# Kernel tuning notes

Measured on AMD Instinct MI355X. Metric: run time of the kernel, lower is better.

## Reference

```python
import jax, jax.numpy as jnp
import numpy as np

B, T_IN, H, IN, OUT, T_DEC = 32768, 20, 128, 2, 2, 45


def lstm_cell(x, h, c, Wih, Whh, bih, bhh):
    # PyTorch gate order: i, f, g, o
    gates = x @ Wih.T + h @ Whh.T + (bih + bhh)
    i, f, g, o = jnp.split(gates, 4, axis=-1)
    c = jax.nn.sigmoid(f) * c + jax.nn.sigmoid(i) * jnp.tanh(g)
    h = jax.nn.sigmoid(o) * jnp.tanh(c)
    return h, c


def lstm_layer(xs, Wih, Whh, bih, bhh):
    # xs: [T, B, in] -> outputs [T, B, H], final (h, c)
    Bsz = xs.shape[1]
    h0 = jnp.zeros((Bsz, H), xs.dtype)
    c0 = jnp.zeros((Bsz, H), xs.dtype)

    def step(carry, x):
        h, c = carry
        h, c = lstm_cell(x, h, c, Wih, Whh, bih, bhh)
        return (h, c), h

    (h, c), ys = jax.lax.scan(step, (h0, c0), xs)
    return ys, h, c


def setup_inputs() -> dict:
    key = jax.random.key(0)
    ks = jax.random.split(key, 20)
    s = 0.05
    d = {
        'input_seq': jax.random.normal(ks[0], (B, T_IN, IN), jnp.float32),
        'enc_Wih0': jax.random.normal(ks[1], (4 * H, IN), jnp.float32) * s,
        'enc_Whh0': jax.random.normal(ks[2], (4 * H, H), jnp.float32) * s,
        'enc_bih0': jax.random.normal(ks[3], (4 * H,), jnp.float32) * s,
        'enc_bhh0': jax.random.normal(ks[4], (4 * H,), jnp.float32) * s,
        'enc_Wih1': jax.random.normal(ks[5], (4 * H, H), jnp.float32) * s,
        'enc_Whh1': jax.random.normal(ks[6], (4 * H, H), jnp.float32) * s,
        'enc_bih1': jax.random.normal(ks[7], (4 * H,), jnp.float32) * s,
        'enc_bhh1': jax.random.normal(ks[8], (4 * H,), jnp.float32) * s,
        'dec_Wih0': jax.random.normal(ks[9], (4 * H, OUT), jnp.float32) * s,
        'dec_Whh0': jax.random.normal(ks[10], (4 * H, H), jnp.float32) * s,
        'dec_bih0': jax.random.normal(ks[11], (4 * H,), jnp.float32) * s,
        'dec_bhh0': jax.random.normal(ks[12], (4 * H,), jnp.float32) * s,
        'dec_Wih1': jax.random.normal(ks[13], (4 * H, H), jnp.float32) * s,
        'dec_Whh1': jax.random.normal(ks[14], (4 * H, H), jnp.float32) * s,
        'dec_bih1': jax.random.normal(ks[15], (4 * H,), jnp.float32) * s,
        'dec_bhh1': jax.random.normal(ks[16], (4 * H,), jnp.float32) * s,
        'fc_W': jax.random.normal(ks[17], (OUT, H), jnp.float32) * s,
        'fc_b': jax.random.normal(ks[18], (OUT,), jnp.float32) * s,
        'target_len': T_DEC,
    }
    return d


def reference(input_seq, enc_Wih0, enc_Whh0, enc_bih0, enc_bhh0,
              enc_Wih1, enc_Whh1, enc_bih1, enc_bhh1,
              dec_Wih0, dec_Whh0, dec_bih0, dec_bhh0,
              dec_Wih1, dec_Whh1, dec_bih1, dec_bhh1,
              fc_W, fc_b, target_len):
    xs = jnp.swapaxes(input_seq, 0, 1)  # [T, B, IN]
    # Encoder: 2 stacked LSTM layers; keep final (h, c) of each layer.
    ys0, h0, c0 = lstm_layer(xs, enc_Wih0, enc_Whh0, enc_bih0, enc_bhh0)
    _, h1, c1 = lstm_layer(ys0, enc_Wih1, enc_Whh1, enc_bih1, enc_bhh1)

    x0 = input_seq[:, -1, :]  # [B, OUT] last observed point

    def dec_step(carry, _):
        hh0, cc0, hh1, cc1, x = carry
        hh0, cc0 = lstm_cell(x, hh0, cc0, dec_Wih0, dec_Whh0, dec_bih0, dec_bhh0)
        hh1, cc1 = lstm_cell(hh0, hh1, cc1, dec_Wih1, dec_Whh1, dec_bih1, dec_bhh1)
        pred = hh1 @ fc_W.T + fc_b  # [B, OUT]
        return (hh0, cc0, hh1, cc1, pred), pred

    _, preds = jax.lax.scan(dec_step, (h0, c0, h1, c1, x0), None, length=target_len)
    return jnp.swapaxes(preds, 0, 1)  # [B, target_len, OUT]
```

## Files before the change

kernel.cpp:

```cpp
#include <hip/hip_runtime.h>

typedef unsigned int u32;
typedef unsigned short u16;
typedef __attribute__((ext_vector_type(8))) short short8;
typedef __attribute__((ext_vector_type(4))) float floatx4;

#define L2E  1.44269504088896340736f
#define L2E2 2.88539008177792681472f

static __device__ __forceinline__ u16 f2bf(float f){
  u32 u = __float_as_uint(f);
  u = (u + 0x7FFFu + ((u >> 16) & 1u)) >> 16;
  return (u16)u;
}
static __device__ __forceinline__ float rcp_(float x){ return __builtin_amdgcn_rcpf(x); }
static __device__ __forceinline__ float exp2_(float x){ return __builtin_amdgcn_exp2f(x); }
static __device__ __forceinline__ float sigm2(float yh){ return rcp_(1.f + exp2_(-yh)); }
static __device__ __forceinline__ float tanh2(float yh2){ return 1.f - 2.f*rcp_(1.f + exp2_(yh2)); }

__global__ __launch_bounds__(256) void prep_weights(
    const float* eWhh0, const float* eWhh1, const float* eWih1,
    const float* dWhh0, const float* dWhh1, const float* dWih1,
    u16* wE0, u16* wE1h, u16* wE1x, u16* wD0, u16* wD1h, u16* wD1x)
{
  int idx = blockIdx.x * 256 + threadIdx.x;
  int m = idx >> 16, e = idx & 65535;
  int j = e & 7, L = (e >> 3) & 63, c = (e >> 9) & 3, g = (e >> 11) & 3, s = (e >> 13) & 7;
  int row = g*128 + s*16 + (L & 15);
  int col = c*32 + ((L >> 4) * 8) + j;
  float scale = (g == 2) ? L2E2 : L2E;
  const float* src; u16* dst;
  switch(m){
    case 0: src = eWhh0; dst = wE0;  break;
    case 1: src = eWhh1; dst = wE1h; break;
    case 2: src = eWih1; dst = wE1x; break;
    case 3: src = dWhh0; dst = wD0;  break;
    case 4: src = dWhh1; dst = wD1h; break;
    default:src = dWih1; dst = wD1x; break;
  }
  dst[e] = f2bf(src[row*128 + col] * scale);
}

__global__ __launch_bounds__(256) void prep_small(
    const float* ebih0,const float* ebhh0,const float* ebih1,const float* ebhh1,
    const float* dbih0,const float* dbhh0,const float* dbih1,const float* dbhh1,
    const float* eWih0,const float* dWih0, float* biasAll, float* wxAll)
{
  int i = blockIdx.x*256 + threadIdx.x;
  if (i < 2048){
    int l = i >> 9, n = i & 511, g = (n >> 7) & 3;
    const float* a = l==0?ebih0: l==1?ebih1: l==2?dbih0: dbih1;
    const float* b = l==0?ebhh0: l==1?ebhh1: l==2?dbhh0: dbhh1;
    biasAll[i] = (a[n] + b[n]) * ((g==2)? L2E2 : L2E);
  } else {
    int k = i - 2048;
    int l = k >> 10, e2 = k & 1023, n = e2 >> 1, g = (n >> 7) & 3;
    const float* wsrc = l ? dWih0 : eWih0;
    wxAll[k] = wsrc[e2] * ((g==2)? L2E2 : L2E);
  }
}

template<bool DEC>
static __device__ __forceinline__ void step_t(
    int grp, int mtb, int lane, int n4, int q, int m0, int t,
    u16* h0s, u16* h1s, float* fcp,
    const float* sB, const float* sWx, const float* sFc,
    const u16* __restrict__ W0, const u16* __restrict__ W1h, const u16* __restrict__ W1x,
    short8 (&ah)[2][4], float2 (&xc)[2][4],
    floatx4 (&c0a)[2][4], floatx4 (&c1a)[2][4],
    float* __restrict__ out)
{
  const int bofs = DEC ? 1024 : 0;
  const int wxo  = DEC ? 512  : 0;

  short8 a1[2][4];
  #pragma unroll
  for (int j = 0; j < 2; j++)
    #pragma unroll
    for (int c = 0; c < 4; c++)
      a1[j][c] = *(const short8*)(h1s + ((mtb+j)*4 + c)*512 + lane*8);

  #pragma unroll 1
  for (int i = 0; i < 4; i++){
    const int s = grp*4 + i;
    const u16* bs = W0 + s*8192;
    short8 bw[4][4];
    #pragma unroll
    for (int c = 0; c < 4; c++)
      #pragma unroll
      for (int g = 0; g < 4; g++)
        bw[g][c] = *(const short8*)(bs + (g*4 + c)*512 + lane*8);
    floatx4 acc[4][2];
    #pragma unroll
    for (int g = 0; g < 4; g++){
      float bi = sB[bofs + g*128 + s*16 + n4];
      float2 wv = ((const float2*)sWx)[wxo + g*128 + s*16 + n4];
      #pragma unroll
      for (int j = 0; j < 2; j++)
        #pragma unroll
        for (int r = 0; r < 4; r++)
          acc[g][j][r] = fmaf(xc[j][r].y, wv.y, fmaf(xc[j][r].x, wv.x, bi));
    }
    #pragma unroll
    for (int c = 0; c < 4; c++)
      #pragma unroll
      for (int g = 0; g < 4; g++){
        acc[g][0] = __builtin_amdgcn_mfma_f32_16x16x32_bf16(ah[0][c], bw[g][c], acc[g][0], 0,0,0);
        acc[g][1] = __builtin_amdgcn_mfma_f32_16x16x32_bf16(ah[1][c], bw[g][c], acc[g][1], 0,0,0);
      }
    #pragma unroll
    for (int j = 0; j < 2; j++){
      const int hb = ((mtb+j)*4 + (s>>1))*512 + ((s&1)*2 + (n4>>3))*128 + q*32 + (n4&7);
      floatx4 cc = c0a[j][i], cn;
      #pragma unroll
      for (int r = 0; r < 4; r++){
        float ig = sigm2(acc[0][j][r]);
        float fg = sigm2(acc[1][j][r]);
        float gg = tanh2(acc[2][j][r]);
        float cv = fmaf(fg, cc[r], ig*gg);
        float og = sigm2(acc[3][j][r]);
        float hv = og * (1.f - 2.f*rcp_(1.f + exp2_(L2E2*cv)));
        cn[r] = cv;
        h0s[hb + r*8] = f2bf(hv);
      }
      c0a[j][i] = cn;
    }
  }
  __syncthreads();

  #pragma unroll
  for (int j = 0; j < 2; j++)
    #pragma unroll
    for (int c = 0; c < 4; c++)
      ah[j][c] = *(const short8*)(h0s + ((mtb+j)*4 + c)*512 + lane*8);

  float p[2][4][2];
  if (DEC){
    #pragma unroll
    for (int j = 0; j < 2; j++)
      #pragma unroll
      for (int r = 0; r < 4; r++){ p[j][r][0] = 0.f; p[j][r][1] = 0.f; }
  }

  #pragma unroll 1
  for (int i = 0; i < 4; i++){
    const int s = grp*4 + i;
    floatx4 acc[4][2];
    #pragma unroll
    for (int g = 0; g < 4; g++){
      float bi = sB[bofs + 512 + g*128 + s*16 + n4];
      #pragma unroll
      for (int j = 0; j < 2; j++)
        #pragma unroll
        for (int r = 0; r < 4; r++) acc[g][j][r] = bi;
    }
    {
      const u16* bs = W1h + s*8192;
      short8 bw[4][4];
      #pragma unroll
      for (int c = 0; c < 4; c++)
        #pragma unroll
        for (int g = 0; g < 4; g++)
          bw[g][c] = *(const short8*)(bs + (g*4 + c)*512 + lane*8);
      #pragma unroll
      for (int c = 0; c < 4; c++)
        #pragma unroll
        for (int g = 0; g < 4; g++){
          acc[g][0] = __builtin_amdgcn_mfma_f32_16x16x32_bf16(a1[0][c], bw[g][c], acc[g][0], 0,0,0);
          acc[g][1] = __builtin_amdgcn_mfma_f32_16x16x32_bf16(a1[1][c], bw[g][c], acc[g][1], 0,0,0);
        }
    }
    {
      const u16* bs = W1x + s*8192;
      short8 bw[4][4];
      #pragma unroll
      for (int c = 0; c < 4; c++)
        #pragma unroll
        for (int g = 0; g < 4; g++)
          bw[g][c] = *(const short8*)(bs + (g*4 + c)*512 + lane*8);
      #pragma unroll
      for (int c = 0; c < 4; c++)
        #pragma unroll
        for (int g = 0; g < 4; g++){
          acc[g][0] = __builtin_amdgcn_mfma_f32_16x16x32_bf16(ah[0][c], bw[g][c], acc[g][0], 0,0,0);
          acc[g][1] = __builtin_amdgcn_mfma_f32_16x16x32_bf16(ah[1][c], bw[g][c], acc[g][1], 0,0,0);
        }
    }
    float f0 = 0.f, f1 = 0.f;
    if (DEC){ f0 = sFc[s*16 + n4]; f1 = sFc[128 + s*16 + n4]; }
    #pragma unroll
    for (int j = 0; j < 2; j++){
      const int hb = ((mtb+j)*4 + (s>>1))*512 + ((s&1)*2 + (n4>>3))*128 + q*32 + (n4&7);
      floatx4 cc = c1a[j][i], cn;
      #pragma unroll
      for (int r = 0; r < 4; r++){
        float ig = sigm2(acc[0][j][r]);
        float fg = sigm2(acc[1][j][r]);
        float gg = tanh2(acc[2][j][r]);
        float cv = fmaf(fg, cc[r], ig*gg);
        float og = sigm2(acc[3][j][r]);
        float hv = og * (1.f - 2.f*rcp_(1.f + exp2_(L2E2*cv)));
        cn[r] = cv;
        h1s[hb + r*8] = f2bf(hv);
        if (DEC){
          p[j][r][0] = fmaf(hv, f0, p[j][r][0]);
          p[j][r][1] = fmaf(hv, f1, p[j][r][1]);
        }
      }
      c1a[j][i] = cn;
    }
  }

  if (DEC){
    #pragma unroll
    for (int off = 1; off < 16; off <<= 1)
      #pragma unroll
      for (int j = 0; j < 2; j++)
        #pragma unroll
        for (int r = 0; r < 4; r++){
          p[j][r][0] += __shfl_xor(p[j][r][0], off);
          p[j][r][1] += __shfl_xor(p[j][r][1], off);
        }
    if (n4 == 0){
      #pragma unroll
      for (int j = 0; j < 2; j++)
        #pragma unroll
        for (int r = 0; r < 4; r++){
          const int base = ((mtb+j)*16 + q*4 + r)*4 + grp*2;
          fcp[base + 0] = p[j][r][0];
          fcp[base + 1] = p[j][r][1];
        }
    }
  }
  __syncthreads();

  if (DEC){
    const float fb0 = sFc[256], fb1 = sFc[257];
    #pragma unroll
    for (int j = 0; j < 2; j++)
      #pragma unroll
      for (int r = 0; r < 4; r++){
        const int base = ((mtb+j)*16 + q*4 + r)*4;
        float2 pv;
        pv.x = fcp[base + 0] + fcp[base + 2] + fb0;
        pv.y = fcp[base + 1] + fcp[base + 3] + fb1;
        xc[j][r] = pv;
        if (grp == 0 && n4 == 0)
          *(float2*)(out + (long)(m0 + (mtb+j)*16 + q*4 + r)*90 + (t - 20)*2) = pv;
      }
  }
}

__global__ __launch_bounds__(512, 1) void lstm_all(
    const float* __restrict__ in_seq,
    const u16* __restrict__ wE0, const u16* __restrict__ wE1h, const u16* __restrict__ wE1x,
    const u16* __restrict__ wD0, const u16* __restrict__ wD1h, const u16* __restrict__ wD1x,
    const float* __restrict__ biasAll, const float* __restrict__ wxAll,
    const float* __restrict__ fcW, const float* __restrict__ fcb,
    float* __restrict__ out)
{
  __shared__ u16 h0s[16384];
  __shared__ u16 h1s[16384];
  __shared__ float sB[2048];
  __shared__ float sWx[2048];
  __shared__ float sFc[260];
  __shared__ float fcp[512];

  const int tid = threadIdx.x, lane = tid & 63, w = tid >> 6;
  const int grp = w >> 2, mtb = (w & 3) * 2;
  const int n4 = lane & 15, q = lane >> 4;
  const int m0 = blockIdx.x * 128;

  for (int i = tid; i < 2048; i += 512){ sB[i] = biasAll[i]; sWx[i] = wxAll[i]; }
  if (tid < 258) sFc[tid] = (tid < 256) ? fcW[tid] : fcb[tid - 256];
  { u32* z0 = (u32*)h0s; u32* z1 = (u32*)h1s;
    for (int i = tid; i < 8192; i += 512){ z0[i] = 0u; z1[i] = 0u; } }

  floatx4 c0a[2][4], c1a[2][4];
  const floatx4 z4 = {0.f,0.f,0.f,0.f};
  #pragma unroll
  for (int j = 0; j < 2; j++)
    #pragma unroll
    for (int i = 0; i < 4; i++){ c0a[j][i] = z4; c1a[j][i] = z4; }
  __syncthreads();

  short8 ah[2][4];
  #pragma unroll
  for (int j = 0; j < 2; j++)
    #pragma unroll
    for (int c = 0; c < 4; c++)
      ah[j][c] = *(const short8*)(h0s + ((mtb+j)*4 + c)*512 + lane*8);
  __syncthreads();

  float2 xc[2][4];

  #pragma unroll 1
  for (int t = 0; t < 20; t++){
    #pragma unroll
    for (int j = 0; j < 2; j++)
      #pragma unroll
      for (int r = 0; r < 4; r++)
        xc[j][r] = *(const float2*)(in_seq + (long)(m0 + (mtb+j)*16 + q*4 + r)*40 + t*2);
    step_t<false>(grp, mtb, lane, n4, q, m0, t, h0s, h1s, fcp, sB, sWx, sFc,
                  wE0, wE1h, wE1x, ah, xc, c0a, c1a, out);
  }

  #pragma unroll
  for (int j = 0; j < 2; j++)
    #pragma unroll
    for (int r = 0; r < 4; r++)
      xc[j][r] = *(const float2*)(in_seq + (long)(m0 + (mtb+j)*16 + q*4 + r)*40 + 38);

  #pragma unroll 1
  for (int t = 20; t < 65; t++){
    step_t<true>(grp, mtb, lane, n4, q, m0, t, h0s, h1s, fcp, sB, sWx, sFc,
                 wD0, wD1h, wD1x, ah, xc, c0a, c1a, out);
  }
}

extern "C" void kernel_launch(void* const* d_in, const int* in_sizes, int n_in,
                              void* d_out, int out_size, void* d_ws, size_t ws_size,
                              hipStream_t stream)
{
  const float* in_seq = (const float*)d_in[0];
  const float* eWih0 = (const float*)d_in[1];
  const float* eWhh0 = (const float*)d_in[2];
  const float* ebih0 = (const float*)d_in[3];
  const float* ebhh0 = (const float*)d_in[4];
  const float* eWih1 = (const float*)d_in[5];
  const float* eWhh1 = (const float*)d_in[6];
  const float* ebih1 = (const float*)d_in[7];
  const float* ebhh1 = (const float*)d_in[8];
  const float* dWih0 = (const float*)d_in[9];
  const float* dWhh0 = (const float*)d_in[10];
  const float* dbih0 = (const float*)d_in[11];
  const float* dbhh0 = (const float*)d_in[12];
  const float* dWih1 = (const float*)d_in[13];
  const float* dWhh1 = (const float*)d_in[14];
  const float* dbih1 = (const float*)d_in[15];
  const float* dbhh1 = (const float*)d_in[16];
  const float* fcW   = (const float*)d_in[17];
  const float* fcb   = (const float*)d_in[18];
  float* out = (float*)d_out;
  char* ws = (char*)d_ws;

  u16* wE0   = (u16*)(ws + 0);
  u16* wE1h  = (u16*)(ws + 131072);
  u16* wE1x  = (u16*)(ws + 262144);
  u16* wD0   = (u16*)(ws + 393216);
  u16* wD1h  = (u16*)(ws + 524288);
  u16* wD1x  = (u16*)(ws + 655360);
  float* biasAll = (float*)(ws + 786432);
  float* wxAll   = (float*)(ws + 794624);

  hipLaunchKernelGGL(prep_weights, dim3(1536), dim3(256), 0, stream,
                     eWhh0, eWhh1, eWih1, dWhh0, dWhh1, dWih1,
                     wE0, wE1h, wE1x, wD0, wD1h, wD1x);
  hipLaunchKernelGGL(prep_small, dim3(16), dim3(256), 0, stream,
                     ebih0, ebhh0, ebih1, ebhh1, dbih0, dbhh0, dbih1, dbhh1,
                     eWih0, dWih0, biasAll, wxAll);

  hipLaunchKernelGGL(lstm_all, dim3(256), dim3(512), 0, stream,
                     in_seq, (const u16*)wE0, (const u16*)wE1h, (const u16*)wE1x,
                     (const u16*)wD0, (const u16*)wD1h, (const u16*)wD1x,
                     (const float*)biasAll, (const float*)wxAll, fcW, fcb, out);
}
```

Baseline: 1.413 ms.

## Software-pipeline weight fragment loads one MFMA block ahead across steps

Measured after the change: 1.705 ms. 1.21x slower.

```diff
diff --git a/kernel.cpp b/kernel.cpp
--- a/kernel.cpp
+++ b/kernel.cpp
@@ -65,31 +65,26 @@
     int grp, int mtb, int lane, int n4, int q, int m0, int t,
     u16* h0s, u16* h1s, float* fcp,
     const float* sB, const float* sWx, const float* sFc,
-    const u16* __restrict__ W0, const u16* __restrict__ W1h, const u16* __restrict__ W1x,
-    short8 (&ah)[2][4], float2 (&xc)[2][4],
+    const u16* __restrict__ W0, const u16* __restrict__ W1h,
+    const u16* __restrict__ W1x, const u16* __restrict__ W0next,
+    short8 (&pf)[16], short8 (&ah)[2][4], float2 (&xc)[2][4],
     floatx4 (&c0a)[2][4], floatx4 (&c1a)[2][4],
     float* __restrict__ out)
 {
   const int bofs = DEC ? 1024 : 0;
   const int wxo  = DEC ? 512  : 0;
+  const int lb = lane * 8;
 
   short8 a1[2][4];
   #pragma unroll
   for (int j = 0; j < 2; j++)
     #pragma unroll
     for (int c = 0; c < 4; c++)
-      a1[j][c] = *(const short8*)(h1s + ((mtb+j)*4 + c)*512 + lane*8);
+      a1[j][c] = *(const short8*)(h1s + ((mtb+j)*4 + c)*512 + lb);
 
   #pragma unroll 1
   for (int i = 0; i < 4; i++){
     const int s = grp*4 + i;
-    const u16* bs = W0 + s*8192;
-    short8 bw[4][4];
-    #pragma unroll
-    for (int c = 0; c < 4; c++)
-      #pragma unroll
-      for (int g = 0; g < 4; g++)
-        bw[g][c] = *(const short8*)(bs + (g*4 + c)*512 + lane*8);
     floatx4 acc[4][2];
     #pragma unroll
     for (int g = 0; g < 4; g++){
@@ -105,9 +100,13 @@
     for (int c = 0; c < 4; c++)
       #pragma unroll
       for (int g = 0; g < 4; g++){
-        acc[g][0] = __builtin_amdgcn_mfma_f32_16x16x32_bf16(ah[0][c], bw[g][c], acc[g][0], 0,0,0);
-        acc[g][1] = __builtin_amdgcn_mfma_f32_16x16x32_bf16(ah[1][c], bw[g][c], acc[g][1], 0,0,0);
-      }
+        acc[g][0] = __builtin_amdgcn_mfma_f32_16x16x32_bf16(ah[0][c], pf[g*4+c], acc[g][0], 0,0,0);
+        acc[g][1] = __builtin_amdgcn_mfma_f32_16x16x32_bf16(ah[1][c], pf[g*4+c], acc[g][1], 0,0,0);
+      }
+    { const u16* nxt = (i < 3) ? (W0 + (s+1)*8192) : (W1h + (grp*4)*8192);
+      #pragma unroll
+      for (int k = 0; k < 16; k++)
+        pf[k] = *(const short8*)(nxt + k*512 + lb); }
     #pragma unroll
     for (int j = 0; j < 2; j++){
       const int hb = ((mtb+j)*4 + (s>>1))*512 + ((s&1)*2 + (n4>>3))*128 + q*32 + (n4&7);
@@ -132,7 +131,7 @@
   for (int j = 0; j < 2; j++)
     #pragma unroll
     for (int c = 0; c < 4; c++)
-      ah[j][c] = *(const short8*)(h0s + ((mtb+j)*4 + c)*512 + lane*8);
+      ah[j][c] = *(const short8*)(h0s + ((mtb+j)*4 + c)*512 + lb);
 
   float p[2][4][2];
   if (DEC){
@@ -154,38 +153,31 @@
         #pragma unroll
         for (int r = 0; r < 4; r++) acc[g][j][r] = bi;
     }
-    {
-      const u16* bs = W1h + s*8192;
-      short8 bw[4][4];
-      #pragma unroll
-      for (int c = 0; c < 4; c++)
-        #pragma unroll
-        for (int g = 0; g < 4; g++)
-          bw[g][c] = *(const short8*)(bs + (g*4 + c)*512 + lane*8);
-      #pragma unroll
-      for (int c = 0; c < 4; c++)
-        #pragma unroll
-        for (int g = 0; g < 4; g++){
-          acc[g][0] = __builtin_amdgcn_mfma_f32_16x16x32_bf16(a1[0][c], bw[g][c], acc[g][0], 0,0,0);
-          acc[g][1] = __builtin_amdgcn_mfma_f32_16x16x32_bf16(a1[1][c], bw[g][c], acc[g][1], 0,0,0);
-        }
-    }
-    {
-      const u16* bs = W1x + s*8192;
-      short8 bw[4][4];
-      #pragma unroll
-      for (int c = 0; c < 4; c++)
-        #pragma unroll
-        for (int g = 0; g < 4; g++)
-          bw[g][c] = *(const short8*)(bs + (g*4 + c)*512 + lane*8);
-      #pragma unroll
-      for (int c = 0; c < 4; c++)
-        #pragma unroll
-        for (int g = 0; g < 4; g++){
-          acc[g][0] = __builtin_amdgcn_mfma_f32_16x16x32_bf16(ah[0][c], bw[g][c], acc[g][0], 0,0,0);
-          acc[g][1] = __builtin_amdgcn_mfma_f32_16x16x32_bf16(ah[1][c], bw[g][c], acc[g][1], 0,0,0);
-        }
-    }
+    #pragma unroll
+    for (int c = 0; c < 4; c++)
+      #pragma unroll
+      for (int g = 0; g < 4; g++){
+        acc[g][0] = __builtin_amdgcn_mfma_f32_16x16x32_bf16(a1[0][c], pf[g*4+c], acc[g][0], 0,0,0);
+        acc[g][1] = __builtin_amdgcn_mfma_f32_16x16x32_bf16(a1[1][c], pf[g*4+c], acc[g][1], 0,0,0);
+      }
+    { const u16* nxt = W1x + s*8192;
+      #pragma unroll
+      for (int k = 0; k < 16; k++)
+        pf[k] = *(const short8*)(nxt + k*512 + lb); }
+    #pragma unroll
+    for (int c = 0; c < 4; c++)
+      #pragma unroll
+      for (int g = 0; g < 4; g++){
+        acc[g][0] = __builtin_amdgcn_mfma_f32_16x16x32_bf16(ah[0][c], pf[g*4+c], acc[g][0], 0,0,0);
+        acc[g][1] = __builtin_amdgcn_mfma_f32_16x16x32_bf16(ah[1][c], pf[g*4+c], acc[g][1], 0,0,0);
+      }
+    { const u16* nxt = (i < 3) ? (W1h + (s+1)*8192)
+                               : (W0next ? (W0next + (grp*4)*8192) : (const u16*)nullptr);
+      if (nxt){
+        #pragma unroll
+        for (int k = 0; k < 16; k++)
+          pf[k] = *(const short8*)(nxt + k*512 + lb);
+      } }
     float f0 = 0.f, f1 = 0.f;
     if (DEC){ f0 = sFc[s*16 + n4]; f1 = sFc[128 + s*16 + n4]; }
     #pragma unroll
@@ -282,6 +274,12 @@
   for (int j = 0; j < 2; j++)
     #pragma unroll
     for (int i = 0; i < 4; i++){ c0a[j][i] = z4; c1a[j][i] = z4; }
+
+  short8 pf[16];
+  { const u16* p0 = wE0 + (grp*4)*8192 + lane*8;
+    #pragma unroll
+    for (int k = 0; k < 16; k++)
+      pf[k] = *(const short8*)(p0 + k*512); }
   __syncthreads();
 
   short8 ah[2][4];
@@ -302,7 +300,8 @@
       for (int r = 0; r < 4; r++)
         xc[j][r] = *(const float2*)(in_seq + (long)(m0 + (mtb+j)*16 + q*4 + r)*40 + t*2);
     step_t<false>(grp, mtb, lane, n4, q, m0, t, h0s, h1s, fcp, sB, sWx, sFc,
-                  wE0, wE1h, wE1x, ah, xc, c0a, c1a, out);
+                  wE0, wE1h, wE1x, (t < 19) ? wE0 : wD0,
+                  pf, ah, xc, c0a, c1a, out);
   }
 
   #pragma unroll
@@ -314,7 +313,8 @@
   #pragma unroll 1
   for (int t = 20; t < 65; t++){
     step_t<true>(grp, mtb, lane, n4, q, m0, t, h0s, h1s, fcp, sB, sWx, sFc,
-                 wD0, wD1h, wD1x, ah, xc, c0a, c1a, out);
+                 wD0, wD1h, wD1x, (t < 64) ? wD0 : (const u16*)nullptr,
+                 pf, ah, xc, c0a, c1a, out);
   }
 }
 
```

## Halve per-block batch tile to 64 rows for higher occupancy

Applied to the files above, without the earlier changes.

After: 2.314 ms. +63.8%, slower.

```diff
diff --git a/kernel.cpp b/kernel.cpp
--- a/kernel.cpp
+++ b/kernel.cpp
@@ -62,152 +62,130 @@
 
 template<bool DEC>
 static __device__ __forceinline__ void step_t(
-    int grp, int mtb, int lane, int n4, int q, int m0, int t,
+    int grp, int mt, int lane, int n4, int q, int m0, int t,
     u16* h0s, u16* h1s, float* fcp,
     const float* sB, const float* sWx, const float* sFc,
-    const u16* __restrict__ W0, const u16* __restrict__ W1h, const u16* __restrict__ W1x,
-    short8 (&ah)[2][4], float2 (&xc)[2][4],
-    floatx4 (&c0a)[2][4], floatx4 (&c1a)[2][4],
+    const u16* __restrict__ W0, const u16* __restrict__ W1h,
+    const u16* __restrict__ W1x,
+    short8 (&ah)[4], float2 (&xc)[4],
+    floatx4 (&c0a)[4], floatx4 (&c1a)[4],
     float* __restrict__ out)
 {
   const int bofs = DEC ? 1024 : 0;
   const int wxo  = DEC ? 512  : 0;
-
-  short8 a1[2][4];
-  #pragma unroll
-  for (int j = 0; j < 2; j++)
-    #pragma unroll
-    for (int c = 0; c < 4; c++)
-      a1[j][c] = *(const short8*)(h1s + ((mtb+j)*4 + c)*512 + lane*8);
+  const int lb = lane * 8;
+
+  short8 a1[4];
+  #pragma unroll
+  for (int c = 0; c < 4; c++)
+    a1[c] = *(const short8*)(h1s + (mt*4 + c)*512 + lb);
 
   #pragma unroll 1
   for (int i = 0; i < 4; i++){
     const int s = grp*4 + i;
     const u16* bs = W0 + s*8192;
-    short8 bw[4][4];
-    #pragma unroll
-    for (int c = 0; c < 4; c++)
-      #pragma unroll
-      for (int g = 0; g < 4; g++)
-        bw[g][c] = *(const short8*)(bs + (g*4 + c)*512 + lane*8);
-    floatx4 acc[4][2];
+    short8 bw[16];
+    #pragma unroll
+    for (int k = 0; k < 16; k++)
+      bw[k] = *(const short8*)(bs + k*512 + lb);
+    floatx4 acc[4];
     #pragma unroll
     for (int g = 0; g < 4; g++){
       float bi = sB[bofs + g*128 + s*16 + n4];
       float2 wv = ((const float2*)sWx)[wxo + g*128 + s*16 + n4];
       #pragma unroll
-      for (int j = 0; j < 2; j++)
-        #pragma unroll
-        for (int r = 0; r < 4; r++)
-          acc[g][j][r] = fmaf(xc[j][r].y, wv.y, fmaf(xc[j][r].x, wv.x, bi));
+      for (int r = 0; r < 4; r++)
+        acc[g][r] = fmaf(xc[r].y, wv.y, fmaf(xc[r].x, wv.x, bi));
     }
     #pragma unroll
     for (int c = 0; c < 4; c++)
       #pragma unroll
-      for (int g = 0; g < 4; g++){
-        acc[g][0] = __builtin_amdgcn_mfma_f32_16x16x32_bf16(ah[0][c], bw[g][c], acc[g][0], 0,0,0);
-        acc[g][1] = __builtin_amdgcn_mfma_f32_16x16x32_bf16(ah[1][c], bw[g][c], acc[g][1], 0,0,0);
-      }
-    #pragma unroll
-    for (int j = 0; j < 2; j++){
-      const int hb = ((mtb+j)*4 + (s>>1))*512 + ((s&1)*2 + (n4>>3))*128 + q*32 + (n4&7);
-      floatx4 cc = c0a[j][i], cn;
+      for (int g = 0; g < 4; g++)
+        acc[g] = __builtin_amdgcn_mfma_f32_16x16x32_bf16(ah[c], bw[g*4+c], acc[g], 0,0,0);
+    {
+      const int hb = (mt*4 + (s>>1))*512 + ((s&1)*2 + (n4>>3))*128 + q*32 + (n4&7);
+      floatx4 cc = c0a[i], cn;
       #pragma unroll
       for (int r = 0; r < 4; r++){
-        float ig = sigm2(acc[0][j][r]);
-        float fg = sigm2(acc[1][j][r]);
-        float gg = tanh2(acc[2][j][r]);
+        float ig = sigm2(acc[0][r]);
+        float fg = sigm2(acc[1][r]);
+        float gg = tanh2(acc[2][r]);
         float cv = fmaf(fg, cc[r], ig*gg);
-        float og = sigm2(acc[3][j][r]);
+        float og = sigm2(acc[3][r]);
         float hv = og * (1.f - 2.f*rcp_(1.f + exp2_(L2E2*cv)));
         cn[r] = cv;
         h0s[hb + r*8] = f2bf(hv);
       }
-      c0a[j][i] = cn;
+      c0a[i] = cn;
     }
   }
   __syncthreads();
 
   #pragma unroll
-  for (int j = 0; j < 2; j++)
-    #pragma unroll
-    for (int c = 0; c < 4; c++)
-      ah[j][c] = *(const short8*)(h0s + ((mtb+j)*4 + c)*512 + lane*8);
-
-  float p[2][4][2];
+  for (int c = 0; c < 4; c++)
+    ah[c] = *(const short8*)(h0s + (mt*4 + c)*512 + lb);
+
+  float p[4][2];
   if (DEC){
     #pragma unroll
-    for (int j = 0; j < 2; j++)
-      #pragma unroll
-      for (int r = 0; r < 4; r++){ p[j][r][0] = 0.f; p[j][r][1] = 0.f; }
+    for (int r = 0; r < 4; r++){ p[r][0] = 0.f; p[r][1] = 0.f; }
   }
 
   #pragma unroll 1
   for (int i = 0; i < 4; i++){
     const int s = grp*4 + i;
-    floatx4 acc[4][2];
+    floatx4 acc[4];
     #pragma unroll
     for (int g = 0; g < 4; g++){
       float bi = sB[bofs + 512 + g*128 + s*16 + n4];
       #pragma unroll
-      for (int j = 0; j < 2; j++)
-        #pragma unroll
-        for (int r = 0; r < 4; r++) acc[g][j][r] = bi;
+      for (int r = 0; r < 4; r++) acc[g][r] = bi;
     }
     {
       const u16* bs = W1h + s*8192;
-      short8 bw[4][4];
+      short8 bw[16];
+      #pragma unroll
+      for (int k = 0; k < 16; k++)
+        bw[k] = *(const short8*)(bs + k*512 + lb);
       #pragma unroll
       for (int c = 0; c < 4; c++)
         #pragma unroll
         for (int g = 0; g < 4; g++)
-          bw[g][c] = *(const short8*)(bs + (g*4 + c)*512 + lane*8);
-      #pragma unroll
-      for (int c = 0; c < 4; c++)
-        #pragma unroll
-        for (int g = 0; g < 4; g++){
-          acc[g][0] = __builtin_amdgcn_mfma_f32_16x16x32_bf16(a1[0][c], bw[g][c], acc[g][0], 0,0,0);
-          acc[g][1] = __builtin_amdgcn_mfma_f32_16x16x32_bf16(a1[1][c], bw[g][c], acc[g][1], 0,0,0);
-        }
+          acc[g] = __builtin_amdgcn_mfma_f32_16x16x32_bf16(a1[c], bw[g*4+c], acc[g], 0,0,0);
     }
     {
       const u16* bs = W1x + s*8192;
-      short8 bw[4][4];
+      short8 bw[16];
+      #pragma unroll
+      for (int k = 0; k < 16; k++)
+        bw[k] = *(const short8*)(bs + k*512 + lb);
       #pragma unroll
       for (int c = 0; c < 4; c++)
         #pragma unroll
         for (int g = 0; g < 4; g++)
-          bw[g][c] = *(const short8*)(bs + (g*4 + c)*512 + lane*8);
-      #pragma unroll
-      for (int c = 0; c < 4; c++)
-        #pragma unroll
-        for (int g = 0; g < 4; g++){
-          acc[g][0] = __builtin_amdgcn_mfma_f32_16x16x32_bf16(ah[0][c], bw[g][c], acc[g][0], 0,0,0);
-          acc[g][1] = __builtin_amdgcn_mfma_f32_16x16x32_bf16(ah[1][c], bw[g][c], acc[g][1], 0,0,0);
-        }
+          acc[g] = __builtin_amdgcn_mfma_f32_16x16x32_bf16(ah[c], bw[g*4+c], acc[g], 0,0,0);
     }
     float f0 = 0.f, f1 = 0.f;
     if (DEC){ f0 = sFc[s*16 + n4]; f1 = sFc[128 + s*16 + n4]; }
-    #pragma unroll
-    for (int j = 0; j < 2; j++){
-      const int hb = ((mtb+j)*4 + (s>>1))*512 + ((s&1)*2 + (n4>>3))*128 + q*32 + (n4&7);
-      floatx4 cc = c1a[j][i], cn;
+    {
+      const int hb = (mt*4 + (s>>1))*512 + ((s&1)*2 + (n4>>3))*128 + q*32 + (n4&7);
+      floatx4 cc = c1a[i], cn;
       #pragma unroll
       for (int r = 0; r < 4; r++){
-        float ig = sigm2(acc[0][j][r]);
-        float fg = sigm2(acc[1][j][r]);
-        float gg = tanh2(acc[2][j][r]);
+        float ig = sigm2(acc[0][r]);
+        float fg = sigm2(acc[1][r]);
+        float gg = tanh2(acc[2][r]);
         float cv = fmaf(fg, cc[r], ig*gg);
-        float og = sigm2(acc[3][j][r]);
+        float og = sigm2(acc[3][r]);
         float hv = og * (1.f - 2.f*rcp_(1.f + exp2_(L2E2*cv)));
         cn[r] = cv;
         h1s[hb + r*8] = f2bf(hv);
         if (DEC){
-          p[j][r][0] = fmaf(hv, f0, p[j][r][0]);
-          p[j][r][1] = fmaf(hv, f1, p[j][r][1]);
+          p[r][0] = fmaf(hv, f0, p[r][0]);
+          p[r][1] = fmaf(hv, f1, p[r][1]);
         }
       }
-      c1a[j][i] = cn;
+      c1a[i] = cn;
     }
   }
 
@@ -215,21 +193,17 @@
     #pragma unroll
     for (int off = 1; off < 16; off <<= 1)
       #pragma unroll
-      for (int j = 0; j < 2; j++)
-        #pragma unroll
-        for (int r = 0; r < 4; r++){
-          p[j][r][0] += __shfl_xor(p[j][r][0], off);
-          p[j][r][1] += __shfl_xor(p[j][r][1], off);
-        }
+      for (int r = 0; r < 4; r++){
+        p[r][0] += __shfl_xor(p[r][0], off);
+        p[r][1] += __shfl_xor(p[r][1], off);
+      }
     if (n4 == 0){
       #pragma unroll
-      for (int j = 0; j < 2; j++)
-        #pragma unroll
-        for (int r = 0; r < 4; r++){
-          const int base = ((mtb+j)*16 + q*4 + r)*4 + grp*2;
-          fcp[base + 0] = p[j][r][0];
-          fcp[base + 1] = p[j][r][1];
-        }
+      for (int r = 0; r < 4; r++){
+        const int base = (mt*16 + q*4 + r)*4 + grp*2;
+        fcp[base + 0] = p[r][0];
+        fcp[base + 1] = p[r][1];
+      }
     }
   }
   __syncthreads();
@@ -237,21 +211,19 @@
   if (DEC){
     const float fb0 = sFc[256], fb1 = sFc[257];
     #pragma unroll
-    for (int j = 0; j < 2; j++)
-      #pragma unroll
-      for (int r = 0; r < 4; r++){
-        const int base = ((mtb+j)*16 + q*4 + r)*4;
-        float2 pv;
-        pv.x = fcp[base + 0] + fcp[base + 2] + fb0;
-        pv.y = fcp[base + 1] + fcp[base + 3] + fb1;
-        xc[j][r] = pv;
-        if (grp == 0 && n4 == 0)
-          *(float2*)(out + (long)(m0 + (mtb+j)*16 + q*4 + r)*90 + (t - 20)*2) = pv;
-      }
-  }
-}
-
-__global__ __launch_bounds__(512, 1) void lstm_all(
+    for (int r = 0; r < 4; r++){
+      const int base = (mt*16 + q*4 + r)*4;
+      float2 pv;
+      pv.x = fcp[base + 0] + fcp[base + 2] + fb0;
+      pv.y = fcp[base + 1] + fcp[base + 3] + fb1;
+      xc[r] = pv;
+      if (grp == 0 && n4 == 0)
+        *(float2*)(out + (long)(m0 + mt*16 + q*4 + r)*90 + (t - 20)*2) = pv;
+    }
+  }
+}
+
+__global__ __launch_bounds__(512, 4) void lstm_all(
     const float* __restrict__ in_seq,
     const u16* __restrict__ wE0, const u16* __restrict__ wE1h, const u16* __restrict__ wE1x,
     const u16* __restrict__ wD0, const u16* __restrict__ wD1h, const u16* __restrict__ wD1x,
@@ -259,61 +231,53 @@
     const float* __restrict__ fcW, const float* __restrict__ fcb,
     float* __restrict__ out)
 {
-  __shared__ u16 h0s[16384];
-  __shared__ u16 h1s[16384];
+  __shared__ u16 h0s[8192];
+  __shared__ u16 h1s[8192];
   __shared__ float sB[2048];
   __shared__ float sWx[2048];
   __shared__ float sFc[260];
-  __shared__ float fcp[512];
+  __shared__ float fcp[256];
 
   const int tid = threadIdx.x, lane = tid & 63, w = tid >> 6;
-  const int grp = w >> 2, mtb = (w & 3) * 2;
+  const int grp = w >> 2, mt = w & 3;
   const int n4 = lane & 15, q = lane >> 4;
-  const int m0 = blockIdx.x * 128;
+  const int m0 = blockIdx.x * 64;
 
   for (int i = tid; i < 2048; i += 512){ sB[i] = biasAll[i]; sWx[i] = wxAll[i]; }
   if (tid < 258) sFc[tid] = (tid < 256) ? fcW[tid] : fcb[tid - 256];
   { u32* z0 = (u32*)h0s; u32* z1 = (u32*)h1s;
-    for (int i = tid; i < 8192; i += 512){ z0[i] = 0u; z1[i] = 0u; } }
-
-  floatx4 c0a[2][4], c1a[2][4];
+    for (int i = tid; i < 4096; i += 512){ z0[i] = 0u; z1[i] = 0u; } }
+
+  floatx4 c0a[4], c1a[4];
   const floatx4 z4 = {0.f,0.f,0.f,0.f};
   #pragma unroll
-  for (int j = 0; j < 2; j++)
-    #pragma unroll
-    for (int i = 0; i < 4; i++){ c0a[j][i] = z4; c1a[j][i] = z4; }
+  for (int i = 0; i < 4; i++){ c0a[i] = z4; c1a[i] = z4; }
   __syncthreads();
 
-  short8 ah[2][4];
-  #pragma unroll
-  for (int j = 0; j < 2; j++)
-    #pragma unroll
-    for (int c = 0; c < 4; c++)
-      ah[j][c] = *(const short8*)(h0s + ((mtb+j)*4 + c)*512 + lane*8);
+  short8 ah[4];
+  #pragma unroll
+  for (int c = 0; c < 4; c++)
+    ah[c] = *(const short8*)(h0s + (mt*4 + c)*512 + lane*8);
   __syncthreads();
 
-  float2 xc[2][4];
+  float2 xc[4];
 
   #pragma unroll 1
   for (int t = 0; t < 20; t++){
     #pragma unroll
-    for (int j = 0; j < 2; j++)
-      #pragma unroll
-      for (int r = 0; r < 4; r++)
-        xc[j][r] = *(const float2*)(in_seq + (long)(m0 + (mtb+j)*16 + q*4 + r)*40 + t*2);
-    step_t<false>(grp, mtb, lane, n4, q, m0, t, h0s, h1s, fcp, sB, sWx, sFc,
+    for (int r = 0; r < 4; r++)
+      xc[r] = *(const float2*)(in_seq + (long)(m0 + mt*16 + q*4 + r)*40 + t*2);
+    step_t<false>(grp, mt, lane, n4, q, m0, t, h0s, h1s, fcp, sB, sWx, sFc,
                   wE0, wE1h, wE1x, ah, xc, c0a, c1a, out);
   }
 
   #pragma unroll
-  for (int j = 0; j < 2; j++)
-    #pragma unroll
-    for (int r = 0; r < 4; r++)
-      xc[j][r] = *(const float2*)(in_seq + (long)(m0 + (mtb+j)*16 + q*4 + r)*40 + 38);
+  for (int r = 0; r < 4; r++)
+    xc[r] = *(const float2*)(in_seq + (long)(m0 + mt*16 + q*4 + r)*40 + 38);
 
   #pragma unroll 1
   for (int t = 20; t < 65; t++){
-    step_t<true>(grp, mtb, lane, n4, q, m0, t, h0s, h1s, fcp, sB, sWx, sFc,
+    step_t<true>(grp, mt, lane, n4, q, m0, t, h0s, h1s, fcp, sB, sWx, sFc,
                  wD0, wD1h, wD1x, ah, xc, c0a, c1a, out);
   }
 }
@@ -360,7 +324,7 @@
                      ebih0, ebhh0, ebih1, ebhh1, dbih0, dbhh0, dbih1, dbhh1,
                      eWih0, dWih0, biasAll, wxAll);
 
-  hipLaunchKernelGGL(lstm_all, dim3(256), dim3(512), 0, stream,
+  hipLaunchKernelGGL(lstm_all, dim3(512), dim3(512), 0, stream,
                      in_seq, (const u16*)wE0, (const u16*)wE1h, (const u16*)wE1x,
                      (const u16*)wD0, (const u16*)wD1h, (const u16*)wD1x,
                      (const float*)biasAll, (const float*)wxAll, fcW, fcb, out);
```
